# Kernel optimization log

Hardware: AMD Instinct MI355X
Metric: run time of the kernel (lower is better)

Reference implementation:

```python
import jax, jax.numpy as jnp
import numpy as np

T, B, D, H = 256, 64, 1024, 1024
G = D + H  # gate input dim (concat of x and hx)


def setup_inputs() -> dict:
    key = jax.random.key(0)
    ks = jax.random.split(key, 5)
    s1 = 1.0 / np.sqrt(G)
    s2 = 1.0 / np.sqrt(H)
    inputs = jax.random.normal(ks[0], (T, B, D), dtype=jnp.float32)
    # gate order along leading axis: forget, input, update, output
    W1 = jax.random.uniform(ks[1], (4, G, H), minval=-s1, maxval=s1, dtype=jnp.float32)
    b1 = jax.random.uniform(ks[2], (4, H), minval=-s1, maxval=s1, dtype=jnp.float32)
    W2 = jax.random.uniform(ks[3], (4, H, H), minval=-s2, maxval=s2, dtype=jnp.float32)
    b2 = jax.random.uniform(ks[4], (4, H), minval=-s2, maxval=s2, dtype=jnp.float32)
    return {"inputs": inputs, "W1": W1, "b1": b1, "W2": W2, "b2": b2}


def reference(inputs, W1, b1, W2, b2):
    # LSTM cell where each gate is: act(Linear2(Linear1(cat[x, h])))
    batch = inputs.shape[1]
    hx0 = jnp.zeros((batch, H), dtype=inputs.dtype)
    cx0 = jnp.zeros((batch, H), dtype=inputs.dtype)

    def step(carry, x):
        hx, cx = carry
        comb = jnp.concatenate([x, hx], axis=1)               # [B, G]
        pre = jnp.einsum('bd,gdh->gbh', comb, W1) + b1[:, None, :]  # [4,B,H]
        z = jnp.einsum('gbh,ghk->gbk', pre, W2) + b2[:, None, :]    # [4,B,H]
        f = jax.nn.sigmoid(z[0])
        i = jax.nn.sigmoid(z[1])
        g = jnp.tanh(z[2])
        o = jax.nn.sigmoid(z[3])
        cx = f * cx + i * g
        hx = o * jnp.tanh(cx)
        return (hx, cx), hx

    (hx, cx), outs = jax.lax.scan(step, (hx0, cx0), inputs)
    return outs, hx, cx
```

## Files before the change

kernel.cpp:

```cpp
#include <hip/hip_runtime.h>
#include <hip/hip_bf16.h>

#define TSTEPS 256
#define NBLK 256

typedef short bf16x8 __attribute__((ext_vector_type(8)));
typedef float f32x4 __attribute__((ext_vector_type(4)));

__device__ __forceinline__ unsigned short f2bf(float f) {
    union { float f; unsigned u; } v; v.f = f;
    unsigned r = v.u + 0x7FFFu + ((v.u >> 16) & 1u);
    return (unsigned short)(r >> 16);
}
__device__ __forceinline__ float bf2f(unsigned short s) {
    union { unsigned u; float f; } v; v.u = ((unsigned)s) << 16; return v.f;
}

__global__ void hq_marker(float* out) { out[0] = 12345.0f; }

__global__ void hq_transpose(const float* __restrict__ in, unsigned short* __restrict__ out) {
    __shared__ float tile[64][65];
    const int R = 1024, C = 1024;
    int r0 = blockIdx.y * 64, c0 = blockIdx.x * 64;
    const float* src = in + (long)blockIdx.z * R * C;
    unsigned short* dst = out + (long)blockIdx.z * R * C;
    int col = threadIdx.x & 63, rr = threadIdx.x >> 6;
#pragma unroll
    for (int i = 0; i < 16; ++i) {
        int row = rr + i * 4;
        tile[row][col] = src[(long)(r0 + row) * C + c0 + col];
    }
    __syncthreads();
#pragma unroll
    for (int i = 0; i < 16; ++i) {
        int row = rr + i * 4;
        dst[(long)(c0 + row) * R + r0 + col] = f2bf(tile[col][row]);
    }
}

__global__ void hq_beff(const unsigned short* __restrict__ w2t, const float* __restrict__ b1,
                        const float* __restrict__ b2, float* __restrict__ beff) {
    int g = blockIdx.y;
    int h = blockIdx.x * 256 + threadIdx.x;
    const unsigned short* row = w2t + ((long)(g * 1024 + h)) * 1024;
    float s = 0.f;
    for (int k = 0; k < 1024; k += 8) {
        bf16x8 v = *reinterpret_cast<const bf16x8*>(row + k);
#pragma unroll
        for (int j = 0; j < 8; ++j) s += bf2f((unsigned short)v[j]) * b1[g * 1024 + k + j];
    }
    beff[g * 1024 + h] = s + b2[g * 1024 + h];
}

__global__ void hq_weff(const unsigned short* __restrict__ w2t, const float* __restrict__ w1,
                        unsigned short* __restrict__ wefft) {
    __shared__ unsigned short atile[64][136];
    const int g = blockIdx.z;
    const int d0 = blockIdx.x * 64;
    const int h0 = blockIdx.y * 64;
    const int tid = threadIdx.x;
    const int w = tid >> 6, lane = tid & 63;
    const int fr = lane & 15, fq = lane >> 4;
    f32x4 acc[4] = {};
    const int drow = d0 + w * 16 + fr;
    const float* bsrc = w1 + ((long)g * 2048 + drow) * 1024;
    for (int kc = 0; kc < 8; ++kc) {
#pragma unroll
        for (int i = 0; i < 4; ++i) {
            int id = tid + i * 256;
            int row = id >> 4, c8 = id & 15;
            bf16x8 v = *reinterpret_cast<const bf16x8*>(
                w2t + ((long)(g * 1024 + h0 + row)) * 1024 + kc * 128 + c8 * 8);
            *reinterpret_cast<bf16x8*>(&atile[row][c8 * 8]) = v;
        }
        __syncthreads();
#pragma unroll
        for (int kk = 0; kk < 4; ++kk) {
            int kl = kk * 32 + fq * 8;
            int kg = kc * 128 + kl;
            float4 bA = *reinterpret_cast<const float4*>(bsrc + kg);
            float4 bB = *reinterpret_cast<const float4*>(bsrc + kg + 4);
            bf16x8 bfv;
            bfv[0] = (short)f2bf(bA.x); bfv[1] = (short)f2bf(bA.y);
            bfv[2] = (short)f2bf(bA.z); bfv[3] = (short)f2bf(bA.w);
            bfv[4] = (short)f2bf(bB.x); bfv[5] = (short)f2bf(bB.y);
            bfv[6] = (short)f2bf(bB.z); bfv[7] = (short)f2bf(bB.w);
#pragma unroll
            for (int mi = 0; mi < 4; ++mi) {
                bf16x8 af = *reinterpret_cast<const bf16x8*>(&atile[mi * 16 + fr][kl]);
                acc[mi] = __builtin_amdgcn_mfma_f32_16x16x32_bf16(af, bfv, acc[mi], 0, 0, 0);
            }
        }
        __syncthreads();
    }
#pragma unroll
    for (int mi = 0; mi < 4; ++mi)
#pragma unroll
        for (int r = 0; r < 4; ++r) {
            int h = h0 + mi * 16 + fq * 4 + r;
            int d = d0 + w * 16 + fr;
            wefft[((long)(g * 1024 + h)) * 2048 + d] = f2bf(acc[mi][r]);
        }
}

__global__ void hq_xconv(const float* __restrict__ x, unsigned short* __restrict__ xbf) {
    long i = (long)blockIdx.x * 256 + threadIdx.x;
    for (; i < 4194304L; i += 524288L) {
        float4 v = reinterpret_cast<const float4*>(x)[i];
        ushort4 o;
        o.x = f2bf(v.x); o.y = f2bf(v.y); o.z = f2bf(v.z); o.w = f2bf(v.w);
        reinterpret_cast<ushort4*>(xbf)[i] = o;
    }
}

__device__ __forceinline__ void coh_load_hx(const void* pa, const void* pb, bf16x8* af) {
    asm volatile(
        "global_load_dwordx4 %0, %[a], off sc0 sc1\n\t"
        "global_load_dwordx4 %1, %[a], off offset:64 sc0 sc1\n\t"
        "global_load_dwordx4 %2, %[a], off offset:128 sc0 sc1\n\t"
        "global_load_dwordx4 %3, %[a], off offset:192 sc0 sc1\n\t"
        "global_load_dwordx4 %4, %[b], off sc0 sc1\n\t"
        "global_load_dwordx4 %5, %[b], off offset:64 sc0 sc1\n\t"
        "global_load_dwordx4 %6, %[b], off offset:128 sc0 sc1\n\t"
        "global_load_dwordx4 %7, %[b], off offset:192 sc0 sc1\n\t"
        "s_waitcnt vmcnt(0)"
        : "=&v"(af[0]), "=&v"(af[1]), "=&v"(af[2]), "=&v"(af[3]),
          "=&v"(af[4]), "=&v"(af[5]), "=&v"(af[6]), "=&v"(af[7])
        : [a] "v"(pa), [b] "v"(pb)
        : "memory");
}
__device__ __forceinline__ unsigned coh_load_flag(const unsigned* p) {
    unsigned r;
    asm volatile(
        "global_load_dword %0, %[a], off sc0 sc1\n\t"
        "s_waitcnt vmcnt(0)"
        : "=&v"(r) : [a] "v"(p) : "memory");
    return r;
}
__device__ __forceinline__ void vm_drain() {
    asm volatile("s_waitcnt vmcnt(0)" ::: "memory");
}
__device__ __forceinline__ void lgkm_barrier() {
    asm volatile("s_waitcnt lgkmcnt(0)\n\ts_barrier" ::: "memory");
    __builtin_amdgcn_sched_barrier(0);
}

__global__ __launch_bounds__(1024, 4) void hq_seq(
    const unsigned short* __restrict__ xbf,
    const unsigned short* __restrict__ wefft,
    const float* __restrict__ beff,
    float* __restrict__ outs,
    float* __restrict__ hxf, float* __restrict__ cxf,
    unsigned short* __restrict__ hxbuf,
    unsigned* __restrict__ flags)
{
    __shared__ float zpart[16][2][32][16];
    __shared__ float hvbuf[256];
    __shared__ float cbuf[256];
    const int tid = threadIdx.x;
    const int lane = tid & 63, kq = tid >> 6;
    const int fr = lane & 15, fq = lane >> 4;
    const int bid = blockIdx.x;
    const int bq = (bid >> 1) & 1;
    const int cb = (bid & 1) | ((bid >> 2) << 1);
    const int b0 = bq * 32, ho = cb * 8;
    const int k0 = kq * 128;
    const int flidx = bq * 128 + cb;

    bf16x8 breg[2][4];
#pragma unroll
    for (int nt = 0; nt < 2; ++nt) {
        const int col = nt * 16 + fr;
        const int g = col >> 3, hl = col & 7;
        const unsigned short* wrow = wefft + ((long)(g * 1024 + ho + hl)) * 2048 + k0 + fq * 8;
#pragma unroll
        for (int s = 0; s < 4; ++s) breg[nt][s] = *(const bf16x8*)(wrow + s * 32);
    }

    const int eb = tid >> 3, ehl = tid & 7;
    float creg = 0.f;
    float be[4] = {0.f, 0.f, 0.f, 0.f};
    if (tid < 256) {
#pragma unroll
        for (int g = 0; g < 4; ++g) be[g] = beff[g * 1024 + ho + ehl];
    }

    const unsigned* my_flag = flags + bq * 128 + ((kq - 8) & 7) * 16 + fr;

    bf16x8 af[8];
    if (kq < 8) {
        const unsigned short* p0 = xbf + ((long)(b0 + fr)) * 1024 + k0 + fq * 8;
        const unsigned short* p1 = p0 + 16 * 1024;
#pragma unroll
        for (int s = 0; s < 4; ++s) {
            af[s]     = *(const bf16x8*)(p0 + s * 32);
            af[4 + s] = *(const bf16x8*)(p1 + s * 32);
        }
    }

    for (int t = 0; t < TSTEPS; ++t) {
        if (kq >= 8) {
            if (t == 0) {
#pragma unroll
                for (int i = 0; i < 8; ++i) af[i] = (bf16x8){0, 0, 0, 0, 0, 0, 0, 0};
            } else {
                for (int g = 0; g < (1 << 16); ++g) {
                    unsigned v = coh_load_flag(my_flag);
                    if (__all(v >= (unsigned)t)) break;
                }
                const unsigned short* hx_r = hxbuf + (t & 1) * 65536;
                const char* pa = (const char*)(hx_r + ((long)(b0 + fr)) * 1024 + (k0 - 1024) + fq * 8);
                const char* pb = pa + 32768;
                coh_load_hx(pa, pb, af);
            }
        }

        f32x4 acc[2][2] = {};
#pragma unroll
        for (int s = 0; s < 4; ++s)
#pragma unroll
            for (int mt = 0; mt < 2; ++mt)
#pragma unroll
                for (int nt = 0; nt < 2; ++nt)
                    acc[mt][nt] = __builtin_amdgcn_mfma_f32_16x16x32_bf16(
                        af[mt * 4 + s], breg[nt][s], acc[mt][nt], 0, 0, 0);

#pragma unroll
        for (int mt = 0; mt < 2; ++mt)
#pragma unroll
            for (int nt = 0; nt < 2; ++nt) {
                const int col = nt * 16 + fr;
                const int prow = (fq * 4) ^ ((col & 3) << 2);
                *(f32x4*)&zpart[kq][mt][col][prow] = acc[mt][nt];
            }
        lgkm_barrier();

        if (tid < 256) {
            const int emt = eb >> 4, erow = eb & 15;
            float z[4];
#pragma unroll
            for (int g = 0; g < 4; ++g) {
                const int col = g * 8 + ehl;
                const int pr = erow ^ ((col & 3) << 2);
                float s = be[g];
#pragma unroll
                for (int q = 0; q < 16; ++q) s += zpart[q][emt][col][pr];
                z[g] = s;
            }
            float fg = 1.f / (1.f + __expf(-z[0]));
            float ig = 1.f / (1.f + __expf(-z[1]));
            float gg = 2.f / (1.f + __expf(-2.f * z[2])) - 1.f;
            float og = 1.f / (1.f + __expf(-z[3]));
            creg = fg * creg + ig * gg;
            float hv = og * (2.f / (1.f + __expf(-2.f * creg)) - 1.f);
            const int b = b0 + eb, h = ho + ehl;
            hvbuf[tid] = hv;
            if (t == TSTEPS - 1) cbuf[tid] = creg;

            unsigned hb = (unsigned)f2bf(hv);
            unsigned ob = (unsigned)__shfl_xor((int)hb, 1);
            if ((tid & 1) == 0) {
                unsigned pack = (hb & 0xFFFFu) | (ob << 16);
                unsigned* hx_w = (unsigned*)(hxbuf + ((t + 1) & 1) * 65536 + b * 1024 + h);
                __hip_atomic_store(hx_w, pack, __ATOMIC_RELAXED, __HIP_MEMORY_SCOPE_AGENT);
            }
            vm_drain();
        }
        lgkm_barrier();
        if (tid == 0)
            __hip_atomic_store(flags + flidx, (unsigned)(t + 1), __ATOMIC_RELAXED,
                               __HIP_MEMORY_SCOPE_AGENT);
        if (kq < 8 && t + 1 < TSTEPS) {
            const unsigned short* p0 = xbf + ((long)((t + 1) * 64 + b0 + fr)) * 1024 + k0 + fq * 8;
            const unsigned short* p1 = p0 + 16 * 1024;
#pragma unroll
            for (int s = 0; s < 4; ++s) {
                af[s]     = *(const bf16x8*)(p0 + s * 32);
                af[4 + s] = *(const bf16x8*)(p1 + s * 32);
            }
        }
        if (tid >= 768) {
            const int et = tid - 768;
            const int b = b0 + (et >> 3), h = ho + (et & 7);
            float hv = hvbuf[et];
            outs[((long)(t * 64 + b)) * 1024 + h] = hv;
            if (t == TSTEPS - 1) { hxf[b * 1024 + h] = hv; cxf[b * 1024 + h] = cbuf[et]; }
        }
    }
}

extern "C" void kernel_launch(void* const* d_in, const int* in_sizes, int n_in,
                              void* d_out, int out_size, void* d_ws, size_t ws_size,
                              hipStream_t stream) {
    (void)in_sizes; (void)n_in; (void)out_size;
    const float* x  = (const float*)d_in[0];
    const float* W1 = (const float*)d_in[1];
    const float* b1 = (const float*)d_in[2];
    const float* W2 = (const float*)d_in[3];
    const float* b2 = (const float*)d_in[4];
    float* outs = (float*)d_out;
    float* hxf = outs + 16777216L;
    float* cxf = hxf + 65536;

    const size_t off_wefft = 0;
    const size_t off_xbf   = 16777216;
    const size_t off_w2t   = off_xbf;
    const size_t off_hx    = 50331648;
    const size_t off_beff  = 50593792;
    const size_t off_flags = 50610176;
    const size_t need      = 50611200;
    if (ws_size < need) { hq_marker<<<1, 1, 0, stream>>>((float*)d_out); return; }

    char* ws = (char*)d_ws;
    unsigned short* wefft = (unsigned short*)(ws + off_wefft);
    unsigned short* xbf   = (unsigned short*)(ws + off_xbf);
    unsigned short* w2t   = (unsigned short*)(ws + off_w2t);
    unsigned short* hxbuf = (unsigned short*)(ws + off_hx);
    float* beff = (float*)(ws + off_beff);
    unsigned* flags = (unsigned*)(ws + off_flags);

    hipMemsetAsync(ws + off_flags, 0, 1024, stream);
    hq_transpose<<<dim3(16, 16, 4), 256, 0, stream>>>(W2, w2t);
    hq_beff<<<dim3(4, 4), 256, 0, stream>>>(w2t, b1, b2, beff);
    hq_weff<<<dim3(32, 16, 4), 256, 0, stream>>>(w2t, W1, wefft);
    hq_xconv<<<2048, 256, 0, stream>>>(x, xbf);

    const unsigned short* xbf_c = xbf;
    const unsigned short* wefft_c = wefft;
    const float* beff_c = beff;
    void* args[] = { (void*)&xbf_c, (void*)&wefft_c, (void*)&beff_c,
                     (void*)&outs, (void*)&hxf, (void*)&cxf,
                     (void*)&hxbuf, (void*)&flags };
    hipError_t ce = hipLaunchCooperativeKernel((const void*)hq_seq, dim3(NBLK), dim3(1024),
                                               args, 0, stream);
    if (ce != hipSuccess) {
        hq_seq<<<NBLK, 1024, 0, stream>>>(xbf, wefft, beff, outs, hxf, cxf, hxbuf, flags);
    }
}
```

Baseline: 1.506 ms.

## Use per-wave sync flags and double-buffer LDS to drop second block barrier

Removes the block-wide barrier after the gate epilogue. Each of the four epilogue waves now publishes its own flag right after draining its hidden-state stores, and consumers poll a 64-lane flag set instead of one flag per block. The z-partials and hidden-value LDS buffers are double-buffered by step parity, and the output write of step t-1 is deferred into step t, so there is no LDS reuse hazard without the barrier. This shortens the per-step critical path of the cross-block recurrence, at the cost of more flag traffic and a larger flag region.

```diff
diff --git a/kernel.cpp b/kernel.cpp
--- a/kernel.cpp
+++ b/kernel.cpp
@@ -152,10 +152,10 @@
     float* __restrict__ outs,
     float* __restrict__ hxf, float* __restrict__ cxf,
     unsigned short* __restrict__ hxbuf,
-    unsigned* __restrict__ flags)
+    unsigned* __restrict__ sflags)
 {
-    __shared__ float zpart[16][2][32][16];
-    __shared__ float hvbuf[256];
+    __shared__ float zpart[2][16][2][32][16];
+    __shared__ float hvbuf[2][256];
     __shared__ float cbuf[256];
     const int tid = threadIdx.x;
     const int lane = tid & 63, kq = tid >> 6;
@@ -165,7 +165,6 @@
     const int cb = (bid & 1) | ((bid >> 2) << 1);
     const int b0 = bq * 32, ho = cb * 8;
     const int k0 = kq * 128;
-    const int flidx = bq * 128 + cb;
 
     bf16x8 breg[2][4];
 #pragma unroll
@@ -185,7 +184,7 @@
         for (int g = 0; g < 4; ++g) be[g] = beff[g * 1024 + ho + ehl];
     }
 
-    const unsigned* my_flag = flags + bq * 128 + ((kq - 8) & 7) * 16 + fr;
+    const unsigned* my_flag = sflags + bq * 512 + ((kq - 8) & 7) * 64 + lane;
 
     bf16x8 af[8];
     if (kq < 8) {
@@ -199,6 +198,7 @@
     }
 
     for (int t = 0; t < TSTEPS; ++t) {
+        const int c = t & 1;
         if (kq >= 8) {
             if (t == 0) {
 #pragma unroll
@@ -231,9 +231,15 @@
             for (int nt = 0; nt < 2; ++nt) {
                 const int col = nt * 16 + fr;
                 const int prow = (fq * 4) ^ ((col & 3) << 2);
-                *(f32x4*)&zpart[kq][mt][col][prow] = acc[mt][nt];
+                *(f32x4*)&zpart[c][kq][mt][col][prow] = acc[mt][nt];
             }
         lgkm_barrier();
+
+        if (tid >= 768 && t > 0) {
+            const int et = tid - 768;
+            const int b = b0 + (et >> 3), h = ho + (et & 7);
+            outs[((long)((t - 1) * 64 + b)) * 1024 + h] = hvbuf[(t - 1) & 1][et];
+        }
 
         if (tid < 256) {
             const int emt = eb >> 4, erow = eb & 15;
@@ -244,7 +250,7 @@
                 const int pr = erow ^ ((col & 3) << 2);
                 float s = be[g];
 #pragma unroll
-                for (int q = 0; q < 16; ++q) s += zpart[q][emt][col][pr];
+                for (int q = 0; q < 16; ++q) s += zpart[c][q][emt][col][pr];
                 z[g] = s;
             }
             float fg = 1.f / (1.f + __expf(-z[0]));
@@ -254,7 +260,7 @@
             creg = fg * creg + ig * gg;
             float hv = og * (2.f / (1.f + __expf(-2.f * creg)) - 1.f);
             const int b = b0 + eb, h = ho + ehl;
-            hvbuf[tid] = hv;
+            hvbuf[t & 1][tid] = hv;
             if (t == TSTEPS - 1) cbuf[tid] = creg;
 
             unsigned hb = (unsigned)f2bf(hv);
@@ -265,11 +271,11 @@
                 __hip_atomic_store(hx_w, pack, __ATOMIC_RELAXED, __HIP_MEMORY_SCOPE_AGENT);
             }
             vm_drain();
-        }
-        lgkm_barrier();
-        if (tid == 0)
-            __hip_atomic_store(flags + flidx, (unsigned)(t + 1), __ATOMIC_RELAXED,
-                               __HIP_MEMORY_SCOPE_AGENT);
+            if (lane == 0)
+                __hip_atomic_store((unsigned*)(sflags + bq * 512 + cb * 4 + kq),
+                                   (unsigned)(t + 1), __ATOMIC_RELAXED,
+                                   __HIP_MEMORY_SCOPE_AGENT);
+        }
         if (kq < 8 && t + 1 < TSTEPS) {
             const unsigned short* p0 = xbf + ((long)((t + 1) * 64 + b0 + fr)) * 1024 + k0 + fq * 8;
             const unsigned short* p1 = p0 + 16 * 1024;
@@ -279,13 +285,15 @@
                 af[4 + s] = *(const bf16x8*)(p1 + s * 32);
             }
         }
-        if (tid >= 768) {
-            const int et = tid - 768;
-            const int b = b0 + (et >> 3), h = ho + (et & 7);
-            float hv = hvbuf[et];
-            outs[((long)(t * 64 + b)) * 1024 + h] = hv;
-            if (t == TSTEPS - 1) { hxf[b * 1024 + h] = hv; cxf[b * 1024 + h] = cbuf[et]; }
-        }
+    }
+    lgkm_barrier();
+    if (tid >= 768) {
+        const int et = tid - 768;
+        const int b = b0 + (et >> 3), h = ho + (et & 7);
+        float hv = hvbuf[1][et];
+        outs[((long)((TSTEPS - 1) * 64 + b)) * 1024 + h] = hv;
+        hxf[b * 1024 + h] = hv;
+        cxf[b * 1024 + h] = cbuf[et];
     }
 }
 
@@ -308,7 +316,7 @@
     const size_t off_hx    = 50331648;
     const size_t off_beff  = 50593792;
     const size_t off_flags = 50610176;
-    const size_t need      = 50611200;
+    const size_t need      = 50614272;
     if (ws_size < need) { hq_marker<<<1, 1, 0, stream>>>((float*)d_out); return; }
 
     char* ws = (char*)d_ws;
@@ -317,9 +325,9 @@
     unsigned short* w2t   = (unsigned short*)(ws + off_w2t);
     unsigned short* hxbuf = (unsigned short*)(ws + off_hx);
     float* beff = (float*)(ws + off_beff);
-    unsigned* flags = (unsigned*)(ws + off_flags);
-
-    hipMemsetAsync(ws + off_flags, 0, 1024, stream);
+    unsigned* sflags = (unsigned*)(ws + off_flags);
+
+    hipMemsetAsync(ws + off_flags, 0, 4096, stream);
     hq_transpose<<<dim3(16, 16, 4), 256, 0, stream>>>(W2, w2t);
     hq_beff<<<dim3(4, 4), 256, 0, stream>>>(w2t, b1, b2, beff);
     hq_weff<<<dim3(32, 16, 4), 256, 0, stream>>>(w2t, W1, wefft);
@@ -330,10 +338,10 @@
     const float* beff_c = beff;
     void* args[] = { (void*)&xbf_c, (void*)&wefft_c, (void*)&beff_c,
                      (void*)&outs, (void*)&hxf, (void*)&cxf,
-                     (void*)&hxbuf, (void*)&flags };
+                     (void*)&hxbuf, (void*)&sflags };
     hipError_t ce = hipLaunchCooperativeKernel((const void*)hq_seq, dim3(NBLK), dim3(1024),
                                                args, 0, stream);
     if (ce != hipSuccess) {
-        hq_seq<<<NBLK, 1024, 0, stream>>>(xbf, wefft, beff, outs, hxf, cxf, hxbuf, flags);
-    }
-}
+        hq_seq<<<NBLK, 1024, 0, stream>>>(xbf, wefft, beff, outs, hxf, cxf, hxbuf, sflags);
+    }
+}
```

After: 1.979 ms. 1.31x slower.
